# Kernel tuning notes

Measured on AMD Instinct MI355X. Metric: run time of the kernel, lower is better.

The kernel has to match this reference:

```python
import jax, jax.numpy as jnp
import numpy as np

B, N, S, K = 16, 16384, 4096, 16
D_PT, D_IN, C_MID, D_OUT = 3, 64, 16, 128
HID = [8, 8]


def _layernorm(x, g, b, eps=1e-5):
    m = x.mean(-1, keepdims=True)
    v = x.var(-1, keepdims=True)
    return (x - m) * jax.lax.rsqrt(v + eps) * g + b


def _gather(feat, idx):
    # feat: [B, C, N], idx: [B, S, K] -> [B, C, S, K]
    return jax.vmap(lambda f, i: f[:, i])(feat, idx)


def setup_inputs() -> dict:
    key = jax.random.key(0)
    ks = jax.random.split(key, 16)
    inp = {
        "xyz": jax.random.normal(ks[0], (B, D_PT, N), jnp.float32),
        "points": jax.random.normal(ks[1], (B, D_IN, N), jnp.float32),
        "new_xyz": jax.random.normal(ks[2], (B, D_PT, S), jnp.float32),
        "nn_idx": jax.random.randint(ks[3], (B, S, K), 0, N, jnp.int32),
    }
    # WeightNet: Linear(3,8)+LN(8), Linear(8,8)+LN(8), Linear(8,16)+LN(16)
    dims = [D_PT] + HID + [C_MID]
    for i in range(3):
        inp[f"w{i}"] = jax.random.normal(ks[4 + i], (dims[i], dims[i + 1]), jnp.float32) * 0.1
        inp[f"b{i}"] = jnp.zeros((dims[i + 1],), jnp.float32)
        inp[f"g{i}"] = jnp.ones((dims[i + 1],), jnp.float32)
        inp[f"be{i}"] = jnp.zeros((dims[i + 1],), jnp.float32)
    last_ch = D_PT + D_IN  # 67
    inp["wl"] = jax.random.normal(ks[8], (C_MID * last_ch, D_OUT), jnp.float32) * 0.02
    inp["bl"] = jnp.zeros((D_OUT,), jnp.float32)
    inp["gl"] = jnp.ones((D_OUT,), jnp.float32)
    inp["bel"] = jnp.zeros((D_OUT,), jnp.float32)
    return inp


def reference(xyz, points, new_xyz, nn_idx,
              w0, b0, g0, be0, w1, b1, g1, be1, w2, b2, g2, be2,
              wl, bl, gl, bel):
    # gather neighbor positions / features: [B, C, S, K]
    grouped_xyz = _gather(xyz, nn_idx)
    gxn = grouped_xyz - new_xyz[:, :, :, None]          # [B, 3, S, K]
    feat = jnp.concatenate([_gather(points, nn_idx), gxn], axis=1)  # [B, 67, S, K]

    # WeightNet on relative coords: MLP over channel dim, layout [B, S, K, 3]
    w = jnp.transpose(gxn, (0, 2, 3, 1))
    for wi, bi, gi, bei in ((w0, b0, g0, be0), (w1, b1, g1, be1), (w2, b2, g2, be2)):
        w = jax.nn.leaky_relu(_layernorm(w @ wi + bi, gi, bei), 0.2)
    # w: [B, S, K, c_mid]

    # weighted aggregation: out[b,s,c,m] = sum_k feat[b,c,s,k] * w[b,s,k,m]
    agg = jnp.einsum("bcsk,bskm->bscm", feat, w).reshape(B, S, -1)  # [B, S, 67*c_mid]

    out = _layernorm(agg @ wl + bl, gl, bel)
    out = jax.nn.leaky_relu(out, 0.2)
    return jnp.transpose(out, (0, 2, 1))  # [B, out_channel, S]
```

## Files before the change

### kernel.cpp

```cpp
#include <hip/hip_runtime.h>

#define B_ 16
#define N_ 16384
#define S_ 4096
#define K_ 16
#define TS 32
#define DOUT 128

typedef __bf16 bf16;
typedef __attribute__((ext_vector_type(8))) __bf16 bf16x8;
typedef __attribute__((ext_vector_type(4))) float f32x4;

__device__ __forceinline__ unsigned pack2(float a, float b) {
  unsigned short ua = __builtin_bit_cast(unsigned short, (bf16)a);
  unsigned short ub = __builtin_bit_cast(unsigned short, (bf16)b);
  return (unsigned)ua | ((unsigned)ub << 16);
}

template <int NCH>
__device__ __forceinline__ void ln_leaky(const float* h, const float* g, const float* e, float* o) {
  float m = 0.f;
#pragma unroll
  for (int j = 0; j < NCH; ++j) m += h[j];
  m *= (1.0f / NCH);
  float v = 0.f;
#pragma unroll
  for (int j = 0; j < NCH; ++j) { float d = h[j] - m; v += d * d; }
  v *= (1.0f / NCH);
  float inv = rsqrtf(v + 1e-5f);
#pragma unroll
  for (int j = 0; j < NCH; ++j) {
    float t = (h[j] - m) * inv * g[j] + e[j];
    o[j] = t < 0.f ? 0.2f * t : t;
  }
}

__global__ void k_fill(float* out, float v) {
  out[blockIdx.x * 256 + threadIdx.x] = v;
}

__global__ __launch_bounds__(256) void k_prep(const float* __restrict__ pts,
                                              bf16* __restrict__ pt,
                                              const float* __restrict__ wl,
                                              bf16* __restrict__ wlF) {
  int bi = blockIdx.x;
  if (bi < 1024) {
    int xcd = bi & 7;
    int li = bi >> 3;
    int b = xcd * 2 + (li >> 6);
    int n0 = (li & 63) * 256;
    int tc = threadIdx.x & 7;
    int tn = threadIdx.x >> 3;
    const float* src = pts + (size_t)b * 64 * N_ + (size_t)(tc * 8) * N_ + n0 + tn * 8;
    float4 row[8][2];
#pragma unroll
    for (int i = 0; i < 8; ++i) {
      row[i][0] = *(const float4*)(src + (size_t)i * N_);
      row[i][1] = *(const float4*)(src + (size_t)i * N_ + 4);
    }
    bf16* dst = pt + ((size_t)b * N_ + n0 + tn * 8) * 64 + tc * 8;
#pragma unroll
    for (int j = 0; j < 8; ++j) {
      float v[8];
#pragma unroll
      for (int i = 0; i < 8; ++i) {
        float4 q = row[i][j >> 2];
        v[i] = ((j & 3) == 0) ? q.x : ((j & 3) == 1) ? q.y : ((j & 3) == 2) ? q.z : q.w;
      }
      *(uint4*)(dst + (size_t)j * 64) = make_uint4(
          pack2(v[0], v[1]), pack2(v[2], v[3]), pack2(v[4], v[5]), pack2(v[6], v[7]));
    }
  } else {
    int blk = bi - 1024;
    int kkg = blk % 34;
    int t = blk / 34;
    int tid = threadIdx.x;
    int L = tid >> 2, jp = (tid & 3) * 2;
    int k = kkg * 32 + ((L >> 4) << 3) + jp;
    int n = t * 16 + (L & 15);
    float v0 = (k < 1072) ? wl[(size_t)k * 128 + n] : 0.f;
    float v1 = (k + 1 < 1072) ? wl[(size_t)(k + 1) * 128 + n] : 0.f;
    ((unsigned*)wlF)[(size_t)blk * 256 + tid] = pack2(v0, v1);
  }
}

__global__ __launch_bounds__(256, 4) void k_main(
    const float* __restrict__ xyz, const float* __restrict__ nxyz,
    const int* __restrict__ nnidx,
    const bf16* __restrict__ ptT, const bf16* __restrict__ wlF,
    const float* __restrict__ w0p, const float* __restrict__ b0p,
    const float* __restrict__ g0p, const float* __restrict__ be0p,
    const float* __restrict__ w1p, const float* __restrict__ b1p,
    const float* __restrict__ g1p, const float* __restrict__ be1p,
    const float* __restrict__ w2p, const float* __restrict__ b2p,
    const float* __restrict__ g2p, const float* __restrict__ be2p,
    const float* __restrict__ blp, const float* __restrict__ glp,
    const float* __restrict__ belp, float* __restrict__ out) {
  __shared__ __align__(16) bf16 w_sT[32 * 264];
  __shared__ __align__(16) bf16 feat2[32 * 144];
  __shared__ __align__(16) bf16 aggA[32 * 136];
  __shared__ float nx[3][TS];
  __shared__ float ln_m[TS], ln_i[TS];

  const int tid = threadIdx.x;
  const unsigned Lwg = blockIdx.y * 128u + blockIdx.x;
  const int xcd = (int)(Lwg & 7u);
  const int li = (int)(Lwg >> 3);
  const int b = xcd * 2 + (li >> 7);
  const int s0 = (li & 127) * TS;
  const size_t ibase = ((size_t)b * S_ + s0) * K_;

  if (tid < 96) {
    int c = tid >> 5, j = tid & 31;
    nx[c][j] = nxyz[((size_t)b * 3 + c) * S_ + s0 + j];
  }
  const int ig0 = nnidx[ibase + tid];
  const int ig1 = nnidx[ibase + tid + 256];
  const int iw0 = nnidx[ibase + 2 * tid];
  const int iw1 = nnidx[ibase + 2 * tid + 1];
  __syncthreads();

  float xa[3], xb[3];
  const int ws = tid >> 3;
  const int wk = (tid & 7) * 2;
  {
#pragma unroll
    for (int c = 0; c < 3; ++c) {
      float nv = nx[c][ws];
      xa[c] = xyz[((size_t)b * 3 + c) * N_ + iw0] - nv;
      xb[c] = xyz[((size_t)b * 3 + c) * N_ + iw1] - nv;
    }
    float ya[8], yb[8];
    {
      float h0[8], h1[8];
#pragma unroll
      for (int j = 0; j < 8; ++j) {
        h0[j] = b0p[j] + xa[0] * w0p[j] + xa[1] * w0p[8 + j] + xa[2] * w0p[16 + j];
        h1[j] = b0p[j] + xb[0] * w0p[j] + xb[1] * w0p[8 + j] + xb[2] * w0p[16 + j];
      }
      ln_leaky<8>(h0, g0p, be0p, ya);
      ln_leaky<8>(h1, g0p, be0p, yb);
    }
    {
      float h0[8], h1[8];
#pragma unroll
      for (int j = 0; j < 8; ++j) { h0[j] = b1p[j]; h1[j] = b1p[j]; }
#pragma unroll
      for (int i = 0; i < 8; ++i) {
#pragma unroll
        for (int j = 0; j < 8; ++j) {
          float w = w1p[i * 8 + j];
          h0[j] += ya[i] * w; h1[j] += yb[i] * w;
        }
      }
      ln_leaky<8>(h0, g1p, be1p, ya);
      ln_leaky<8>(h1, g1p, be1p, yb);
    }
    {
      float h0[16], h1[16];
#pragma unroll
      for (int j = 0; j < 16; ++j) { h0[j] = b2p[j]; h1[j] = b2p[j]; }
#pragma unroll
      for (int i = 0; i < 8; ++i) {
#pragma unroll
        for (int j = 0; j < 16; ++j) {
          float w = w2p[i * 16 + j];
          h0[j] += ya[i] * w; h1[j] += yb[i] * w;
        }
      }
      float z0[16], z1[16];
      ln_leaky<16>(h0, g2p, be2p, z0);
      ln_leaky<16>(h1, g2p, be2p, z1);
      bf16* wp = w_sT + ws * 264 + wk;
#pragma unroll
      for (int m = 0; m < 16; ++m)
        *(unsigned*)(wp + m * 16) = pack2(z0[m], z1[m]);
    }
  }

  const int lane = tid & 63;
  const int wv = tid >> 6;
  const int l16 = lane & 15;
  const int q = lane >> 4;
  const bool adiag = ((((lane >> 5) ^ (lane >> 3)) & 1) == 0);
  const int aoff = ((lane >> 3) & 1) * 144 + (lane & 7) * 16 + (q & 1) * 8;
  const int boff = (lane >> 5) * 264 + l16 * 16 + (q & 1) * 8;
  const int soff = (lane >> 5) * 136 + (q & 1) * 64 + l16;
  f32x4 a00 = {0.f, 0.f, 0.f, 0.f};
  f32x4 a01 = a00, a10 = a00, a11 = a00;
  const f32x4 zc = a00;

  const bf16* ptB = ptT + (size_t)b * N_ * 64;
  const int gs0 = tid >> 4, gk = tid & 15;

  uint4 pf0, pf1;
  pf0 = *(const uint4*)(ptB + (size_t)ig0 * 64);
  pf1 = *(const uint4*)(ptB + (size_t)ig1 * 64);

  for (int ch = 0; ch < 9; ++ch) {
    const int nkk = (ch < 8) ? 4 : 2;
    __syncthreads();
    if (ch < 8) {
      bf16 t0[8], t1[8];
      *(uint4*)t0 = pf0;
      *(uint4*)t1 = pf1;
      bf16* f0 = feat2 + gs0 * 144 + gk;
      bf16* f1 = feat2 + (gs0 + 16) * 144 + gk;
#pragma unroll
      for (int c = 0; c < 8; ++c) {
        f0[c * 16] = t0[c];
        f1[c * 16] = t1[c];
      }
    } else {
      bf16* fp = feat2 + ws * 144 + wk;
      *(unsigned*)(fp + 0 * 16) = pack2(xa[0], xb[0]);
      *(unsigned*)(fp + 1 * 16) = pack2(xa[1], xb[1]);
      *(unsigned*)(fp + 2 * 16) = pack2(xa[2], xb[2]);
#pragma unroll
      for (int c = 3; c < 8; ++c) *(unsigned*)(fp + c * 16) = 0u;
    }
    __syncthreads();
    if (ch < 8) {
      int nc = ch + 1;
      if (nc < 8) {
        pf0 = *(const uint4*)(ptB + (size_t)ig0 * 64 + nc * 8);
        pf1 = *(const uint4*)(ptB + (size_t)ig1 * 64 + nc * 8);
      }
    }
#pragma unroll
    for (int pp = 0; pp < 4; ++pp) {
      int s2 = (wv * 4 + pp) * 2;
      uint4 au = *(const uint4*)(feat2 + s2 * 144 + aoff);
      if (!adiag) au = make_uint4(0u, 0u, 0u, 0u);
      bf16x8 af = __builtin_bit_cast(bf16x8, au);
      bf16x8 bw = *(const bf16x8*)(w_sT + s2 * 264 + boff);
      f32x4 d = __builtin_amdgcn_mfma_f32_16x16x32_bf16(af, bw, zc, 0, 0, 0);
      bf16* cp = aggA + s2 * 136 + soff;
#pragma unroll
      for (int r = 0; r < 4; ++r) cp[r * 16] = (bf16)d[r];
    }
    __syncthreads();
    {
      const bf16* arow0 = aggA + l16 * 136 + q * 8;
      const bf16* arow1 = aggA + (16 + l16) * 136 + q * 8;
      const size_t lb = (size_t)lane * 8;
      const size_t kb = (size_t)(ch * 4) * 512;
      const bf16* w0f = wlF + (size_t)wv * 17408 + kb + lb;
      const bf16* w1f = wlF + (size_t)(wv + 4) * 17408 + kb + lb;
      for (int kk = 0; kk < nkk; ++kk) {
        bf16x8 af0 = *(const bf16x8*)(arow0 + kk * 32);
        bf16x8 af1 = *(const bf16x8*)(arow1 + kk * 32);
        bf16x8 bf0 = *(const bf16x8*)(w0f + kk * 512);
        bf16x8 bf1 = *(const bf16x8*)(w1f + kk * 512);
        a00 = __builtin_amdgcn_mfma_f32_16x16x32_bf16(af0, bf0, a00, 0, 0, 0);
        a01 = __builtin_amdgcn_mfma_f32_16x16x32_bf16(af0, bf1, a01, 0, 0, 0);
        a10 = __builtin_amdgcn_mfma_f32_16x16x32_bf16(af1, bf0, a10, 0, 0, 0);
        a11 = __builtin_amdgcn_mfma_f32_16x16x32_bf16(af1, bf1, a11, 0, 0, 0);
      }
    }
  }

  __syncthreads();
  float* out_s = (float*)w_sT;
  {
    int row0 = q * 4;
    int row1 = 16 + q * 4;
    int c0 = wv * 16 + l16;
    int c1 = 64 + c0;
    float bl0 = blp[c0], bl1 = blp[c1];
#pragma unroll
    for (int r = 0; r < 4; ++r) {
      out_s[(row0 + r) * 132 + c0] = a00[r] + bl0;
      out_s[(row0 + r) * 132 + c1] = a01[r] + bl1;
      out_s[(row1 + r) * 132 + c0] = a10[r] + bl0;
      out_s[(row1 + r) * 132 + c1] = a11[r] + bl1;
    }
  }
  __syncthreads();
  {
    int r = tid >> 3, g = tid & 7;
    const float* rowp = out_s + r * 132;
    float s1 = 0.f;
#pragma unroll
    for (int i = 0; i < 16; ++i) s1 += rowp[g + 8 * i];
    s1 += __shfl_xor(s1, 1);
    s1 += __shfl_xor(s1, 2);
    s1 += __shfl_xor(s1, 4);
    float m = s1 * (1.0f / 128.0f);
    float s2 = 0.f;
#pragma unroll
    for (int i = 0; i < 16; ++i) { float d = rowp[g + 8 * i] - m; s2 += d * d; }
    s2 += __shfl_xor(s2, 1);
    s2 += __shfl_xor(s2, 2);
    s2 += __shfl_xor(s2, 4);
    if (g == 0) {
      ln_m[r] = m;
      ln_i[r] = rsqrtf(s2 * (1.0f / 128.0f) + 1e-5f);
    }
  }
  __syncthreads();
  {
    int d = tid >> 1, sh = tid & 1;
    float gld = glp[d], beld = belp[d];
    float vals[16];
#pragma unroll
    for (int j = 0; j < 16; ++j) {
      int r = sh * 16 + j;
      float v = (out_s[r * 132 + d] - ln_m[r]) * ln_i[r] * gld + beld;
      vals[j] = v < 0.f ? 0.2f * v : v;
    }
    float* op = out + ((size_t)b * DOUT + d) * S_ + s0 + sh * 16;
#pragma unroll
    for (int i = 0; i < 4; ++i)
      *(float4*)(op + 4 * i) =
          make_float4(vals[4 * i], vals[4 * i + 1], vals[4 * i + 2], vals[4 * i + 3]);
  }
}

extern "C" void kernel_launch(void* const* d_in, const int* in_sizes, int n_in,
                              void* d_out, int out_size, void* d_ws, size_t ws_size,
                              hipStream_t stream) {
  const float* xyz  = (const float*)d_in[0];
  const float* pts  = (const float*)d_in[1];
  const float* nxyz = (const float*)d_in[2];
  const int* nnidx  = (const int*)d_in[3];
  const float* w0p  = (const float*)d_in[4];
  const float* b0p  = (const float*)d_in[5];
  const float* g0p  = (const float*)d_in[6];
  const float* be0p = (const float*)d_in[7];
  const float* w1p  = (const float*)d_in[8];
  const float* b1p  = (const float*)d_in[9];
  const float* g1p  = (const float*)d_in[10];
  const float* be1p = (const float*)d_in[11];
  const float* w2p  = (const float*)d_in[12];
  const float* b2p  = (const float*)d_in[13];
  const float* g2p  = (const float*)d_in[14];
  const float* be2p = (const float*)d_in[15];
  const float* wlp  = (const float*)d_in[16];
  const float* blp  = (const float*)d_in[17];
  const float* glp  = (const float*)d_in[18];
  const float* belp = (const float*)d_in[19];
  float* out = (float*)d_out;

  const size_t PTT_BYTES = (size_t)B_ * N_ * 64 * 2;
  const size_t WLF_BYTES = (size_t)8 * 34 * 64 * 8 * 2;
  bf16* ptT = (bf16*)d_ws;
  bf16* wlF = (bf16*)((char*)d_ws + PTT_BYTES);

  (void)hipGetLastError();

  if (ws_size < PTT_BYTES + WLF_BYTES) {
    k_fill<<<dim3(8), dim3(256), 0, stream>>>(out, 5000.0f);
    return;
  }

  k_prep<<<dim3(1024 + 8 * 34), dim3(256), 0, stream>>>(pts, ptT, wlp, wlF);
  hipError_t e1 = hipGetLastError();
  k_main<<<dim3(S_ / TS, B_), dim3(256), 0, stream>>>(
      xyz, nxyz, nnidx, ptT, wlF,
      w0p, b0p, g0p, be0p, w1p, b1p, g1p, be1p,
      w2p, b2p, g2p, be2p, blp, glp, belp, out);
  hipError_t e3 = hipGetLastError();

  if (e1 != hipSuccess)
    k_fill<<<dim3(8), dim3(256), 0, stream>>>(out, 2000.0f + (float)(int)e1);
  if (e3 != hipSuccess)
    k_fill<<<dim3(8), dim3(256), 0, stream>>>(out, 4000.0f + (float)(int)e3);
}
```

Measured before the change: 231.0 us.

## Double threads per block to 512, one neighbor per thread

Doubles the block size of the main kernel from 256 to 512 threads so each thread handles a single neighbor (gather, WeightNet MLP, feature staging) instead of two. The final GEMM is split across 8 waves as 2 row tiles by 4 column tiles, and the LayerNorm and output stages are re-partitioned to match. The aim is more parallelism for latency-bound gathers and less per-thread register pressure. In exchange there are more threads per barrier, narrower bf16 stores to LDS, and a launch bound of (512,8) that limits registers per thread.

Measured after the change: 243.4 us. 1.05x slower.

```diff
diff --git a/kernel.cpp b/kernel.cpp
--- a/kernel.cpp
+++ b/kernel.cpp
@@ -84,7 +84,7 @@
   }
 }
 
-__global__ __launch_bounds__(256, 4) void k_main(
+__global__ __launch_bounds__(512, 8) void k_main(
     const float* __restrict__ xyz, const float* __restrict__ nxyz,
     const int* __restrict__ nnidx,
     const bf16* __restrict__ ptT, const bf16* __restrict__ wlF,
@@ -114,122 +114,93 @@
     int c = tid >> 5, j = tid & 31;
     nx[c][j] = nxyz[((size_t)b * 3 + c) * S_ + s0 + j];
   }
-  const int ig0 = nnidx[ibase + tid];
-  const int ig1 = nnidx[ibase + tid + 256];
-  const int iw0 = nnidx[ibase + 2 * tid];
-  const int iw1 = nnidx[ibase + 2 * tid + 1];
+  const int ig = nnidx[ibase + tid];
+  const int ps = tid >> 4;
+  const int pk = tid & 15;
+
+  const bf16* ptB = ptT + (size_t)b * N_ * 64;
+  uint4 pf = *(const uint4*)(ptB + (size_t)ig * 64);
   __syncthreads();
 
-  float xa[3], xb[3];
-  const int ws = tid >> 3;
-  const int wk = (tid & 7) * 2;
+  float xa[3];
   {
 #pragma unroll
-    for (int c = 0; c < 3; ++c) {
-      float nv = nx[c][ws];
-      xa[c] = xyz[((size_t)b * 3 + c) * N_ + iw0] - nv;
-      xb[c] = xyz[((size_t)b * 3 + c) * N_ + iw1] - nv;
-    }
-    float ya[8], yb[8];
+    for (int c = 0; c < 3; ++c)
+      xa[c] = xyz[((size_t)b * 3 + c) * N_ + ig] - nx[c][ps];
+    float ya[8];
     {
-      float h0[8], h1[8];
-#pragma unroll
-      for (int j = 0; j < 8; ++j) {
+      float h0[8];
+#pragma unroll
+      for (int j = 0; j < 8; ++j)
         h0[j] = b0p[j] + xa[0] * w0p[j] + xa[1] * w0p[8 + j] + xa[2] * w0p[16 + j];
-        h1[j] = b0p[j] + xb[0] * w0p[j] + xb[1] * w0p[8 + j] + xb[2] * w0p[16 + j];
-      }
       ln_leaky<8>(h0, g0p, be0p, ya);
-      ln_leaky<8>(h1, g0p, be0p, yb);
     }
     {
-      float h0[8], h1[8];
-#pragma unroll
-      for (int j = 0; j < 8; ++j) { h0[j] = b1p[j]; h1[j] = b1p[j]; }
+      float h0[8];
+#pragma unroll
+      for (int j = 0; j < 8; ++j) h0[j] = b1p[j];
 #pragma unroll
       for (int i = 0; i < 8; ++i) {
 #pragma unroll
-        for (int j = 0; j < 8; ++j) {
-          float w = w1p[i * 8 + j];
-          h0[j] += ya[i] * w; h1[j] += yb[i] * w;
-        }
+        for (int j = 0; j < 8; ++j) h0[j] += ya[i] * w1p[i * 8 + j];
       }
       ln_leaky<8>(h0, g1p, be1p, ya);
-      ln_leaky<8>(h1, g1p, be1p, yb);
     }
     {
-      float h0[16], h1[16];
-#pragma unroll
-      for (int j = 0; j < 16; ++j) { h0[j] = b2p[j]; h1[j] = b2p[j]; }
+      float h0[16];
+#pragma unroll
+      for (int j = 0; j < 16; ++j) h0[j] = b2p[j];
 #pragma unroll
       for (int i = 0; i < 8; ++i) {
 #pragma unroll
-        for (int j = 0; j < 16; ++j) {
-          float w = w2p[i * 16 + j];
-          h0[j] += ya[i] * w; h1[j] += yb[i] * w;
-        }
+        for (int j = 0; j < 16; ++j) h0[j] += ya[i] * w2p[i * 16 + j];
       }
-      float z0[16], z1[16];
+      float z0[16];
       ln_leaky<16>(h0, g2p, be2p, z0);
-      ln_leaky<16>(h1, g2p, be2p, z1);
-      bf16* wp = w_sT + ws * 264 + wk;
-#pragma unroll
-      for (int m = 0; m < 16; ++m)
-        *(unsigned*)(wp + m * 16) = pack2(z0[m], z1[m]);
+      bf16* wp = w_sT + ps * 264 + pk;
+#pragma unroll
+      for (int m = 0; m < 16; ++m) wp[m * 16] = (bf16)z0[m];
     }
   }
 
   const int lane = tid & 63;
   const int wv = tid >> 6;
+  const int rt = wv & 1;
+  const int ct = wv >> 1;
   const int l16 = lane & 15;
   const int q = lane >> 4;
   const bool adiag = ((((lane >> 5) ^ (lane >> 3)) & 1) == 0);
   const int aoff = ((lane >> 3) & 1) * 144 + (lane & 7) * 16 + (q & 1) * 8;
   const int boff = (lane >> 5) * 264 + l16 * 16 + (q & 1) * 8;
   const int soff = (lane >> 5) * 136 + (q & 1) * 64 + l16;
-  f32x4 a00 = {0.f, 0.f, 0.f, 0.f};
-  f32x4 a01 = a00, a10 = a00, a11 = a00;
-  const f32x4 zc = a00;
-
-  const bf16* ptB = ptT + (size_t)b * N_ * 64;
-  const int gs0 = tid >> 4, gk = tid & 15;
-
-  uint4 pf0, pf1;
-  pf0 = *(const uint4*)(ptB + (size_t)ig0 * 64);
-  pf1 = *(const uint4*)(ptB + (size_t)ig1 * 64);
+  f32x4 a0 = {0.f, 0.f, 0.f, 0.f};
+  f32x4 a1 = a0;
+  const f32x4 zc = a0;
+
+  bf16* fdst = feat2 + ps * 144 + pk;
 
   for (int ch = 0; ch < 9; ++ch) {
     const int nkk = (ch < 8) ? 4 : 2;
     __syncthreads();
     if (ch < 8) {
-      bf16 t0[8], t1[8];
-      *(uint4*)t0 = pf0;
-      *(uint4*)t1 = pf1;
-      bf16* f0 = feat2 + gs0 * 144 + gk;
-      bf16* f1 = feat2 + (gs0 + 16) * 144 + gk;
-#pragma unroll
-      for (int c = 0; c < 8; ++c) {
-        f0[c * 16] = t0[c];
-        f1[c * 16] = t1[c];
-      }
+      bf16 t0[8];
+      *(uint4*)t0 = pf;
+#pragma unroll
+      for (int c = 0; c < 8; ++c) fdst[c * 16] = t0[c];
     } else {
-      bf16* fp = feat2 + ws * 144 + wk;
-      *(unsigned*)(fp + 0 * 16) = pack2(xa[0], xb[0]);
-      *(unsigned*)(fp + 1 * 16) = pack2(xa[1], xb[1]);
-      *(unsigned*)(fp + 2 * 16) = pack2(xa[2], xb[2]);
-#pragma unroll
-      for (int c = 3; c < 8; ++c) *(unsigned*)(fp + c * 16) = 0u;
+      fdst[0 * 16] = (bf16)xa[0];
+      fdst[1 * 16] = (bf16)xa[1];
+      fdst[2 * 16] = (bf16)xa[2];
+#pragma unroll
+      for (int c = 3; c < 8; ++c) fdst[c * 16] = (bf16)0.f;
     }
     __syncthreads();
-    if (ch < 8) {
-      int nc = ch + 1;
-      if (nc < 8) {
-        pf0 = *(const uint4*)(ptB + (size_t)ig0 * 64 + nc * 8);
-        pf1 = *(const uint4*)(ptB + (size_t)ig1 * 64 + nc * 8);
-      }
-    }
-#pragma unroll
-    for (int pp = 0; pp < 4; ++pp) {
-      int s2 = (wv * 4 + pp) * 2;
+    if (ch < 7) {
+      pf = *(const uint4*)(ptB + (size_t)ig * 64 + (ch + 1) * 8);
+    }
+#pragma unroll
+    for (int pp = 0; pp < 2; ++pp) {
+      int s2 = wv * 4 + pp * 2;
       uint4 au = *(const uint4*)(feat2 + s2 * 144 + aoff);
       if (!adiag) au = make_uint4(0u, 0u, 0u, 0u);
       bf16x8 af = __builtin_bit_cast(bf16x8, au);
@@ -241,21 +212,17 @@
     }
     __syncthreads();
     {
-      const bf16* arow0 = aggA + l16 * 136 + q * 8;
-      const bf16* arow1 = aggA + (16 + l16) * 136 + q * 8;
+      const bf16* arow = aggA + (rt * 16 + l16) * 136 + q * 8;
       const size_t lb = (size_t)lane * 8;
       const size_t kb = (size_t)(ch * 4) * 512;
-      const bf16* w0f = wlF + (size_t)wv * 17408 + kb + lb;
-      const bf16* w1f = wlF + (size_t)(wv + 4) * 17408 + kb + lb;
+      const bf16* w0f = wlF + (size_t)ct * 17408 + kb + lb;
+      const bf16* w1f = wlF + (size_t)(ct + 4) * 17408 + kb + lb;
       for (int kk = 0; kk < nkk; ++kk) {
-        bf16x8 af0 = *(const bf16x8*)(arow0 + kk * 32);
-        bf16x8 af1 = *(const bf16x8*)(arow1 + kk * 32);
+        bf16x8 af = *(const bf16x8*)(arow + kk * 32);
         bf16x8 bf0 = *(const bf16x8*)(w0f + kk * 512);
         bf16x8 bf1 = *(const bf16x8*)(w1f + kk * 512);
-        a00 = __builtin_amdgcn_mfma_f32_16x16x32_bf16(af0, bf0, a00, 0, 0, 0);
-        a01 = __builtin_amdgcn_mfma_f32_16x16x32_bf16(af0, bf1, a01, 0, 0, 0);
-        a10 = __builtin_amdgcn_mfma_f32_16x16x32_bf16(af1, bf0, a10, 0, 0, 0);
-        a11 = __builtin_amdgcn_mfma_f32_16x16x32_bf16(af1, bf1, a11, 0, 0, 0);
+        a0 = __builtin_amdgcn_mfma_f32_16x16x32_bf16(af, bf0, a0, 0, 0, 0);
+        a1 = __builtin_amdgcn_mfma_f32_16x16x32_bf16(af, bf1, a1, 0, 0, 0);
       }
     }
   }
@@ -263,36 +230,35 @@
   __syncthreads();
   float* out_s = (float*)w_sT;
   {
-    int row0 = q * 4;
-    int row1 = 16 + q * 4;
-    int c0 = wv * 16 + l16;
+    int row = rt * 16 + q * 4;
+    int c0 = ct * 16 + l16;
     int c1 = 64 + c0;
     float bl0 = blp[c0], bl1 = blp[c1];
 #pragma unroll
     for (int r = 0; r < 4; ++r) {
-      out_s[(row0 + r) * 132 + c0] = a00[r] + bl0;
-      out_s[(row0 + r) * 132 + c1] = a01[r] + bl1;
-      out_s[(row1 + r) * 132 + c0] = a10[r] + bl0;
-      out_s[(row1 + r) * 132 + c1] = a11[r] + bl1;
+      out_s[(row + r) * 132 + c0] = a0[r] + bl0;
+      out_s[(row + r) * 132 + c1] = a1[r] + bl1;
     }
   }
   __syncthreads();
   {
-    int r = tid >> 3, g = tid & 7;
+    int r = tid >> 4, g = tid & 15;
     const float* rowp = out_s + r * 132;
     float s1 = 0.f;
 #pragma unroll
-    for (int i = 0; i < 16; ++i) s1 += rowp[g + 8 * i];
+    for (int i = 0; i < 8; ++i) s1 += rowp[g + 16 * i];
     s1 += __shfl_xor(s1, 1);
     s1 += __shfl_xor(s1, 2);
     s1 += __shfl_xor(s1, 4);
+    s1 += __shfl_xor(s1, 8);
     float m = s1 * (1.0f / 128.0f);
     float s2 = 0.f;
 #pragma unroll
-    for (int i = 0; i < 16; ++i) { float d = rowp[g + 8 * i] - m; s2 += d * d; }
+    for (int i = 0; i < 8; ++i) { float d = rowp[g + 16 * i] - m; s2 += d * d; }
     s2 += __shfl_xor(s2, 1);
     s2 += __shfl_xor(s2, 2);
     s2 += __shfl_xor(s2, 4);
+    s2 += __shfl_xor(s2, 8);
     if (g == 0) {
       ln_m[r] = m;
       ln_i[r] = rsqrtf(s2 * (1.0f / 128.0f) + 1e-5f);
@@ -300,20 +266,18 @@
   }
   __syncthreads();
   {
-    int d = tid >> 1, sh = tid & 1;
+    int d = tid >> 2, sh = tid & 3;
     float gld = glp[d], beld = belp[d];
-    float vals[16];
-#pragma unroll
-    for (int j = 0; j < 16; ++j) {
-      int r = sh * 16 + j;
+    float vals[8];
+#pragma unroll
+    for (int j = 0; j < 8; ++j) {
+      int r = sh * 8 + j;
       float v = (out_s[r * 132 + d] - ln_m[r]) * ln_i[r] * gld + beld;
       vals[j] = v < 0.f ? 0.2f * v : v;
     }
-    float* op = out + ((size_t)b * DOUT + d) * S_ + s0 + sh * 16;
-#pragma unroll
-    for (int i = 0; i < 4; ++i)
-      *(float4*)(op + 4 * i) =
-          make_float4(vals[4 * i], vals[4 * i + 1], vals[4 * i + 2], vals[4 * i + 3]);
+    float* op = out + ((size_t)b * DOUT + d) * S_ + s0 + sh * 8;
+    *(float4*)(op + 0) = make_float4(vals[0], vals[1], vals[2], vals[3]);
+    *(float4*)(op + 4) = make_float4(vals[4], vals[5], vals[6], vals[7]);
   }
 }
 
@@ -356,7 +320,7 @@
 
   k_prep<<<dim3(1024 + 8 * 34), dim3(256), 0, stream>>>(pts, ptT, wlp, wlF);
   hipError_t e1 = hipGetLastError();
-  k_main<<<dim3(S_ / TS, B_), dim3(256), 0, stream>>>(
+  k_main<<<dim3(S_ / TS, B_), dim3(512), 0, stream>>>(
       xyz, nxyz, nnidx, ptT, wlF,
       w0p, b0p, g0p, be0p, w1p, b1p, g1p, be1p,
       w2p, b2p, g2p, be2p, blp, glp, belp, out);
```

## Repack wl and agg layouts so LDS stores are packed 32-bit writes

Applied to the files above, without the earlier changes.

The K ordering of the aggregation matrix changes so each thread writes pairs of MFMA outputs as packed 32-bit words into a wider-strided aggA. The wl prepacking permutation is updated to match. The feature gather now reuses the per-thread neighbour indices iw0/iw1, so the transposed LDS writes become packed 32-bit stores instead of scalar 16-bit ones, and two index loads are dropped. The aim is to cut LDS store count and bank conflicts, at the cost of more shared memory and a layout that must match exactly across the prepack and main kernels.

New measurement: 231.8 us. No clear change (+0.4%).

```diff
diff --git a/kernel.cpp b/kernel.cpp
--- a/kernel.cpp
+++ b/kernel.cpp
@@ -76,10 +76,13 @@
     int t = blk / 34;
     int tid = threadIdx.x;
     int L = tid >> 2, jp = (tid & 3) * 2;
-    int k = kkg * 32 + ((L >> 4) << 3) + jp;
+    int p0 = ((L >> 4) << 3) + jp;
+    int m = p0 >> 1;
+    int c0 = kkg * 2;
+    int c1 = c0 + 1;
     int n = t * 16 + (L & 15);
-    float v0 = (k < 1072) ? wl[(size_t)k * 128 + n] : 0.f;
-    float v1 = (k + 1 < 1072) ? wl[(size_t)(k + 1) * 128 + n] : 0.f;
+    float v0 = (c0 < 67) ? wl[(size_t)(c0 * 16 + m) * 128 + n] : 0.f;
+    float v1 = (c1 < 67) ? wl[(size_t)(c1 * 16 + m) * 128 + n] : 0.f;
     ((unsigned*)wlF)[(size_t)blk * 256 + tid] = pack2(v0, v1);
   }
 }
@@ -98,7 +101,7 @@
     const float* __restrict__ belp, float* __restrict__ out) {
   __shared__ __align__(16) bf16 w_sT[32 * 264];
   __shared__ __align__(16) bf16 feat2[32 * 144];
-  __shared__ __align__(16) bf16 aggA[32 * 136];
+  __shared__ __align__(16) bf16 aggA[32 * 160];
   __shared__ float nx[3][TS];
   __shared__ float ln_m[TS], ln_i[TS];
 
@@ -114,8 +117,6 @@
     int c = tid >> 5, j = tid & 31;
     nx[c][j] = nxyz[((size_t)b * 3 + c) * S_ + s0 + j];
   }
-  const int ig0 = nnidx[ibase + tid];
-  const int ig1 = nnidx[ibase + tid + 256];
   const int iw0 = nnidx[ibase + 2 * tid];
   const int iw1 = nnidx[ibase + 2 * tid + 1];
   __syncthreads();
@@ -185,31 +186,29 @@
   const bool adiag = ((((lane >> 5) ^ (lane >> 3)) & 1) == 0);
   const int aoff = ((lane >> 3) & 1) * 144 + (lane & 7) * 16 + (q & 1) * 8;
   const int boff = (lane >> 5) * 264 + l16 * 16 + (q & 1) * 8;
-  const int soff = (lane >> 5) * 136 + (q & 1) * 64 + l16;
+  const int cdw = ((q & 1) << 5) + l16;
   f32x4 a00 = {0.f, 0.f, 0.f, 0.f};
   f32x4 a01 = a00, a10 = a00, a11 = a00;
   const f32x4 zc = a00;
 
   const bf16* ptB = ptT + (size_t)b * N_ * 64;
-  const int gs0 = tid >> 4, gk = tid & 15;
 
   uint4 pf0, pf1;
-  pf0 = *(const uint4*)(ptB + (size_t)ig0 * 64);
-  pf1 = *(const uint4*)(ptB + (size_t)ig1 * 64);
+  pf0 = *(const uint4*)(ptB + (size_t)iw0 * 64);
+  pf1 = *(const uint4*)(ptB + (size_t)iw1 * 64);
 
   for (int ch = 0; ch < 9; ++ch) {
     const int nkk = (ch < 8) ? 4 : 2;
     __syncthreads();
     if (ch < 8) {
-      bf16 t0[8], t1[8];
-      *(uint4*)t0 = pf0;
-      *(uint4*)t1 = pf1;
-      bf16* f0 = feat2 + gs0 * 144 + gk;
-      bf16* f1 = feat2 + (gs0 + 16) * 144 + gk;
-#pragma unroll
-      for (int c = 0; c < 8; ++c) {
-        f0[c * 16] = t0[c];
-        f1[c * 16] = t1[c];
+      const unsigned* a4 = (const unsigned*)&pf0;
+      const unsigned* b4 = (const unsigned*)&pf1;
+      unsigned* fb = (unsigned*)(feat2 + ws * 144 + wk);
+#pragma unroll
+      for (int w = 0; w < 4; ++w) {
+        unsigned a = a4[w], bb = b4[w];
+        fb[(2 * w) * 8] = (a & 0xffffu) | (bb << 16);
+        fb[(2 * w + 1) * 8] = (a >> 16) | (bb & 0xffff0000u);
       }
     } else {
       bf16* fp = feat2 + ws * 144 + wk;
@@ -220,12 +219,9 @@
       for (int c = 3; c < 8; ++c) *(unsigned*)(fp + c * 16) = 0u;
     }
     __syncthreads();
-    if (ch < 8) {
-      int nc = ch + 1;
-      if (nc < 8) {
-        pf0 = *(const uint4*)(ptB + (size_t)ig0 * 64 + nc * 8);
-        pf1 = *(const uint4*)(ptB + (size_t)ig1 * 64 + nc * 8);
-      }
+    if (ch < 7) {
+      pf0 = *(const uint4*)(ptB + (size_t)iw0 * 64 + (ch + 1) * 8);
+      pf1 = *(const uint4*)(ptB + (size_t)iw1 * 64 + (ch + 1) * 8);
     }
 #pragma unroll
     for (int pp = 0; pp < 4; ++pp) {
@@ -235,14 +231,14 @@
       bf16x8 af = __builtin_bit_cast(bf16x8, au);
       bf16x8 bw = *(const bf16x8*)(w_sT + s2 * 264 + boff);
       f32x4 d = __builtin_amdgcn_mfma_f32_16x16x32_bf16(af, bw, zc, 0, 0, 0);
-      bf16* cp = aggA + s2 * 136 + soff;
-#pragma unroll
-      for (int r = 0; r < 4; ++r) cp[r * 16] = (bf16)d[r];
+      unsigned* cw = (unsigned*)(aggA + (size_t)(s2 + (lane >> 5)) * 160);
+      cw[cdw] = pack2(d[0], d[1]);
+      cw[cdw + 16] = pack2(d[2], d[3]);
     }
     __syncthreads();
     {
-      const bf16* arow0 = aggA + l16 * 136 + q * 8;
-      const bf16* arow1 = aggA + (16 + l16) * 136 + q * 8;
+      const bf16* arow0 = aggA + l16 * 160 + q * 8;
+      const bf16* arow1 = aggA + (16 + l16) * 160 + q * 8;
       const size_t lb = (size_t)lane * 8;
       const size_t kb = (size_t)(ch * 4) * 512;
       const bf16* w0f = wlF + (size_t)wv * 17408 + kb + lb;
```
